# Performance work log

Hardware: AMD Instinct MI355X
Metric: run time of the kernel (lower is better)

Reference implementation:

```python
import jax, jax.numpy as jnp
import numpy as np

D = 1024      # hidden_size
FF = 4096     # ff_inner_dim = 4 * D
E = 8         # num_experts
K = 2         # moe_top_k
B, L = 4, 1024


def setup_inputs() -> dict:
    key = jax.random.key(0)
    ks = jax.random.split(key, 12)
    s = 0.02  # weight init scale
    return {
        "x": jax.random.normal(ks[0], (B, L, D), jnp.float32),
        "W_gate": jax.random.normal(ks[1], (D, E), jnp.float32) * s,
        "W1": jax.random.normal(ks[2], (E, D, FF), jnp.float32) * s,
        "b1": jnp.zeros((E, FF), jnp.float32),
        "W2": jax.random.normal(ks[3], (E, FF, D), jnp.float32) * s,
        "b2": jnp.zeros((E, D), jnp.float32),
        "Ws1": jax.random.normal(ks[4], (D, FF), jnp.float32) * s,
        "bs1": jnp.zeros((FF,), jnp.float32),
        "Ws2": jax.random.normal(ks[5], (FF, D), jnp.float32) * s,
        "bs2": jnp.zeros((D,), jnp.float32),
    }


def _gelu(h):
    # torch F.gelu default = exact (erf) gelu
    return jax.nn.gelu(h, approximate=False)


def reference(x, W_gate, W1, b1, W2, b2, Ws1, bs1, Ws2, bs2):
    Bx, Lx, Dx = x.shape
    xf = x.reshape(-1, Dx)                       # [T, D]
    logits = xf @ W_gate                         # [T, E]
    probs = jax.nn.softmax(logits, axis=-1)
    top_v, top_i = jax.lax.top_k(probs, K)       # [T, K]
    top_v = top_v / jnp.sum(top_v, axis=-1, keepdims=True)
    # dense combine weights: [T, E], zero for unselected experts
    combine = jnp.sum(jax.nn.one_hot(top_i, E, dtype=xf.dtype) * top_v[..., None], axis=1)

    out = jnp.zeros_like(xf)
    for e in range(E):  # fixed small expert loop, unrolled under jit
        h = _gelu(xf @ W1[e] + b1[e])            # [T, FF]
        out = out + combine[:, e:e + 1] * (h @ W2[e] + b2[e])

    shared = _gelu(xf @ Ws1 + bs1) @ Ws2 + bs2   # [T, D]
    return (out + shared).reshape(Bx, Lx, Dx)
```

## Files before the change

### kernel.cpp

```cpp
#include <hip/hip_runtime.h>
#include <hip/hip_bf16.h>

typedef unsigned short ushort_t;
typedef __attribute__((ext_vector_type(4))) float f32x4;
typedef __attribute__((ext_vector_type(8))) short bf16x8;
typedef __attribute__((ext_vector_type(8))) unsigned short us8;

#define T_TOK 4096
#define D_DIM 1024
#define FF_DIM 4096
#define NE 8
#define ESTRIDE 4194304L

__device__ __forceinline__ unsigned short f2bf(float f) {
  __hip_bfloat16 h = __float2bfloat16(f);
  return __builtin_bit_cast(unsigned short, h);
}
__device__ __forceinline__ float gelu_f(float v) {
  return 0.5f * v * (1.0f + erff(v * 0.70710678118654752440f));
}

__global__ void gate_kernel(const float* __restrict__ x, const float* __restrict__ Wg,
                            int* __restrict__ cnt, int* __restrict__ tok,
                            float* __restrict__ wof, int* __restrict__ rankof) {
  const int t = blockIdx.x;
  const int lane = threadIdx.x;
  const float* xr = x + (long)t * D_DIM;
  float acc[NE];
#pragma unroll
  for (int e = 0; e < NE; e++) acc[e] = 0.f;
#pragma unroll
  for (int i = 0; i < 16; i++) {
    int d = i * 64 + lane;
    float xv = xr[d];
    const float* wr = Wg + d * NE;
#pragma unroll
    for (int e = 0; e < NE; e++) acc[e] += xv * wr[e];
  }
#pragma unroll
  for (int off = 32; off > 0; off >>= 1) {
#pragma unroll
    for (int e = 0; e < NE; e++) acc[e] += __shfl_xor(acc[e], off, 64);
  }
  if (lane == 0) {
    int i0 = 0;
#pragma unroll
    for (int e = 1; e < NE; e++) if (acc[e] > acc[i0]) i0 = e;
    int i1 = -1;
#pragma unroll
    for (int e = 0; e < NE; e++) {
      if (e == i0) continue;
      if (i1 < 0 || acc[e] > acc[i1]) i1 = e;
    }
    float e1 = expf(acc[i1] - acc[i0]);
    float w0 = 1.f / (1.f + e1);
    float w1 = e1 * w0;
    int s0 = atomicAdd(&cnt[i0], 1);
    tok[i0 * T_TOK + s0] = t; wof[i0 * T_TOK + s0] = w0; rankof[i0 * T_TOK + s0] = 0;
    int s1 = atomicAdd(&cnt[i1], 1);
    tok[i1 * T_TOK + s1] = t; wof[i1 * T_TOK + s1] = w1; rankof[i1 * T_TOK + s1] = 1;
    tok[8 * T_TOK + t] = t; wof[8 * T_TOK + t] = 1.f; rankof[8 * T_TOK + t] = 0;
  }
}

__global__ void scan_kernel(int* cnt, int* base) {
  if (threadIdx.x == 0 && blockIdx.x == 0) {
    int s = 0;
    for (int e = 0; e < NE; e++) { base[e] = s; s += cnt[e]; }
    base[8] = s;
    cnt[8] = T_TOK;
  }
}

__global__ void build_queue_kernel(const int* __restrict__ cnt,
                                   unsigned int* __restrict__ q1,
                                   unsigned int* __restrict__ q2,
                                   int* __restrict__ nq) {
  const int e = blockIdx.x;
  int off1 = 0, off2 = 0, tot1 = 0, tot2 = 0, mym = 0;
  for (int i = 0; i < 9; i++) {
    int c = (i == 8) ? T_TOK : cnt[i];
    int m = (c + 127) >> 7;
    if (i < e) { off1 += m * 32; off2 += m * 8; }
    if (i == e) mym = m;
    tot1 += m * 32; tot2 += m * 8;
  }
  for (int nx = 0; nx < 32; nx++)
    for (int my = threadIdx.x; my < mym; my += 256)
      q1[off1 + nx * mym + my] = ((unsigned)e << 16) | ((unsigned)my << 8) | (unsigned)nx;
  for (int nx = 0; nx < 8; nx++)
    for (int my = threadIdx.x; my < mym; my += 256)
      q2[off2 + nx * mym + my] = ((unsigned)e << 16) | ((unsigned)my << 8) | (unsigned)nx;
  if (e == 0 && threadIdx.x == 0) { nq[0] = tot1; nq[1] = tot2; }
}

__global__ void cvt_x_kernel(const float* __restrict__ src, ushort_t* __restrict__ dst) {
  long i = ((long)blockIdx.x * 256 + threadIdx.x) * 8;
  float4 v0 = *(const float4*)(src + i);
  float4 v1 = *(const float4*)(src + i + 4);
  us8 o;
  o[0] = f2bf(v0.x); o[1] = f2bf(v0.y); o[2] = f2bf(v0.z); o[3] = f2bf(v0.w);
  o[4] = f2bf(v1.x); o[5] = f2bf(v1.y); o[6] = f2bf(v1.z); o[7] = f2bf(v1.w);
  *(us8*)(dst + i) = o;
}

__global__ void tcvt_kernel(const float* __restrict__ src, ushort_t* __restrict__ dst,
                            int R, int C) {
  src += (long)blockIdx.z * R * C;
  dst += (long)blockIdx.z * R * C;
  const int r0 = blockIdx.y * 64, c0 = blockIdx.x * 64;
  __shared__ ushort_t tile[64][72];
  const int t = threadIdx.x;
#pragma unroll
  for (int i = 0; i < 4; i++) {
    int lin = t + i * 256;
    int r = lin >> 4;
    int c = (lin & 15) * 4;
    float4 v = *(const float4*)(src + (long)(r0 + r) * C + c0 + c);
    tile[c + 0][r] = f2bf(v.x);
    tile[c + 1][r] = f2bf(v.y);
    tile[c + 2][r] = f2bf(v.z);
    tile[c + 3][r] = f2bf(v.w);
  }
  __syncthreads();
#pragma unroll
  for (int i = 0; i < 2; i++) {
    int lin = t + i * 256;
    int cc = lin >> 3, rp = lin & 7;
    us8 v = *(const us8*)&tile[cc][rp * 8];
    *(us8*)(dst + (long)(c0 + cc) * R + r0 + rp * 8) = v;
  }
}

template <int K, int N, int PHASE>
__global__ __launch_bounds__(256, 3) void gemm_kernel(
    const ushort_t* __restrict__ Abase, const ushort_t* __restrict__ WT,
    const float* __restrict__ bias_e, const float* __restrict__ bias_s,
    const int* __restrict__ cnt, const int* __restrict__ base,
    const int* __restrict__ tok, const float* __restrict__ wof,
    const int* __restrict__ rankof,
    const unsigned int* __restrict__ q, const int* __restrict__ nq_all,
    ushort_t* __restrict__ He, float* __restrict__ ybuf, float* __restrict__ out) {
  const int nq = nq_all[PHASE - 1];
  const int tid = threadIdx.x;
  const int w = tid >> 6, lane = tid & 63;
  const int wm = w >> 1, wn = w & 1;
  const int lr = lane & 15, lg = lane >> 4;

  __shared__ ushort_t lds_u[2 * 8192];
  char* const lds = (char*)lds_u;

  const int srow8 = tid >> 3;
  const int g8 = (tid & 7) ^ (srow8 & 7);

  int offA[4], offB[4];
#pragma unroll
  for (int m = 0; m < 4; m++) {
    int r = wm * 64 + m * 16 + lr;
    offA[m] = r * 128 + ((lg ^ (r & 7)) << 4);
  }
#pragma unroll
  for (int n = 0; n < 4; n++) {
    int r = wn * 64 + n * 16 + lr;
    offB[n] = r * 128 + ((lg ^ (r & 7)) << 4);
  }

  for (int it = blockIdx.x; it < nq; it += gridDim.x) {
    const unsigned int item = q[it];
    const int e = item >> 16;
    const int m0 = ((item >> 8) & 0xff) * 128;
    const int n0 = (item & 0xff) * 128;
    const int count = cnt[e];

    const ushort_t* pA[4];
    const ushort_t* pB[4];
#pragma unroll
    for (int i = 0; i < 4; i++) {
      int rr = m0 + i * 32 + srow8;
      int rc = (rr < count) ? rr : 0;
      long arow;
      if (PHASE == 1) arow = tok[e * T_TOK + rc];
      else            arow = (long)base[e] + rc;
      pA[i] = Abase + arow * (long)K + g8 * 8;
      pB[i] = WT + (long)e * ESTRIDE + (long)(n0 + i * 32 + srow8) * K + g8 * 8;
    }

    f32x4 acc[4][4] = {};

    for (int k0 = 0; k0 < K; k0 += 64) {
#pragma unroll
      for (int i = 0; i < 4; i++) {
        __builtin_amdgcn_global_load_lds(
            (const __attribute__((address_space(1))) void*)(pA[i] + k0),
            (__attribute__((address_space(3))) void*)(lds + i * 4096 + tid * 16), 16, 0, 0);
        __builtin_amdgcn_global_load_lds(
            (const __attribute__((address_space(1))) void*)(pB[i] + k0),
            (__attribute__((address_space(3))) void*)(lds + 16384 + i * 4096 + tid * 16),
            16, 0, 0);
      }
      __syncthreads();

#pragma unroll
      for (int kk = 0; kk < 2; kk++) {
        const int kx = kk << 6;
        bf16x8 av[4], bv[4];
#pragma unroll
        for (int m = 0; m < 4; m++)
          av[m] = *(const bf16x8*)(lds + (offA[m] ^ kx));
#pragma unroll
        for (int n = 0; n < 4; n++)
          bv[n] = *(const bf16x8*)(lds + 16384 + (offB[n] ^ kx));
#pragma unroll
        for (int m = 0; m < 4; m++)
#pragma unroll
          for (int n = 0; n < 4; n++)
            acc[m][n] = __builtin_amdgcn_mfma_f32_16x16x32_bf16(av[m], bv[n], acc[m][n], 0, 0, 0);
      }
      __syncthreads();
    }

    const float* bias = (e == NE) ? bias_s : (bias_e + (long)e * N);
#pragma unroll
    for (int m = 0; m < 4; m++) {
#pragma unroll
      for (int j = 0; j < 4; j++) {
        int rloc = wm * 64 + m * 16 + lg * 4 + j;
        int rr = m0 + rloc;
        if (rr >= count) continue;
        if (PHASE == 1) {
          long orow = (long)base[e] + rr;
#pragma unroll
          for (int n = 0; n < 4; n++) {
            int col = n0 + wn * 64 + n * 16 + lr;
            float v = acc[m][n][j] + bias[col];
            He[orow * FF_DIM + col] = f2bf(gelu_f(v));
          }
        } else {
          int tt = tok[e * T_TOK + rr];
          if (e == NE) {
#pragma unroll
            for (int n = 0; n < 4; n++) {
              int col = n0 + wn * 64 + n * 16 + lr;
              out[(long)tt * D_DIM + col] = acc[m][n][j] + bias[col];
            }
          } else {
            float wgt = wof[e * T_TOK + rr];
            int rk = rankof[e * T_TOK + rr];
            float* dst = ybuf + (long)rk * ((long)T_TOK * D_DIM) + (long)tt * D_DIM;
#pragma unroll
            for (int n = 0; n < 4; n++) {
              int col = n0 + wn * 64 + n * 16 + lr;
              dst[col] = wgt * (acc[m][n][j] + bias[col]);
            }
          }
        }
      }
    }
  }
}

__global__ void final_add_kernel(float* __restrict__ out, const float* __restrict__ ybuf) {
  long i = ((long)blockIdx.x * 256 + threadIdx.x) * 4;
  float4 a = *(const float4*)(out + i);
  float4 b = *(const float4*)(ybuf + i);
  float4 c = *(const float4*)(ybuf + (long)T_TOK * D_DIM + i);
  a.x += b.x + c.x; a.y += b.y + c.y; a.z += b.z + c.z; a.w += b.w + c.w;
  *(float4*)(out + i) = a;
}

extern "C" void kernel_launch(void* const* d_in, const int* in_sizes, int n_in,
                              void* d_out, int out_size, void* d_ws, size_t ws_size,
                              hipStream_t stream) {
  (void)in_sizes; (void)n_in; (void)out_size; (void)ws_size;
  const float* x   = (const float*)d_in[0];
  const float* Wg  = (const float*)d_in[1];
  const float* W1  = (const float*)d_in[2];
  const float* b1  = (const float*)d_in[3];
  const float* W2  = (const float*)d_in[4];
  const float* b2  = (const float*)d_in[5];
  const float* Ws1 = (const float*)d_in[6];
  const float* bs1 = (const float*)d_in[7];
  const float* Ws2 = (const float*)d_in[8];
  const float* bs2 = (const float*)d_in[9];
  float* out = (float*)d_out;

  char* ws = (char*)d_ws;
  int*      cnt    = (int*)(ws + 0);
  int*      base   = (int*)(ws + 64);
  int*      tok    = (int*)(ws + 256);
  float*    wof    = (float*)(ws + 256 + 147456);
  int*      rankof = (int*)(ws + 256 + 2 * 147456);
  ushort_t* Xbf    = (ushort_t*)(ws + 442624);
  ushort_t* W1T    = (ushort_t*)(ws + 8831232);
  ushort_t* W2T    = (ushort_t*)(ws + 84328704);
  ushort_t* He     = (ushort_t*)(ws + 159826176);
  int*      nq     = (int*)(ws + 260489472);
  unsigned int* q1 = (unsigned int*)(ws + 260489536);
  unsigned int* q2 = (unsigned int*)(ws + 260489536 + 32768);
  float*    ybuf   = (float*)(ws + 261538048);

  hipMemsetAsync(cnt, 0, 64, stream);
  gate_kernel<<<T_TOK, 64, 0, stream>>>(x, Wg, cnt, tok, wof, rankof);
  scan_kernel<<<1, 64, 0, stream>>>(cnt, base);
  build_queue_kernel<<<9, 256, 0, stream>>>(cnt, q1, q2, nq);
  cvt_x_kernel<<<2048, 256, 0, stream>>>(x, Xbf);
  tcvt_kernel<<<dim3(64, 16, 8), 256, 0, stream>>>(W1, W1T, 1024, 4096);
  tcvt_kernel<<<dim3(16, 64, 8), 256, 0, stream>>>(W2, W2T, 4096, 1024);
  tcvt_kernel<<<dim3(64, 16, 1), 256, 0, stream>>>(Ws1, W1T + 8L * ESTRIDE, 1024, 4096);
  tcvt_kernel<<<dim3(16, 64, 1), 256, 0, stream>>>(Ws2, W2T + 8L * ESTRIDE, 4096, 1024);
  gemm_kernel<1024, 4096, 1><<<3328, 256, 0, stream>>>(
      Xbf, W1T, b1, bs1, cnt, base, tok, wof, rankof, q1, nq, He, ybuf, out);
  gemm_kernel<4096, 1024, 2><<<832, 256, 0, stream>>>(
      He, W2T, b2, bs2, cnt, base, tok, wof, rankof, q2, nq, He, ybuf, out);
  final_add_kernel<<<4096, 256, 0, stream>>>(out, ybuf);
}
```

Baseline: 603.9 us.

## Double-buffer GEMM LDS loads, swizzle tile queue, merge weight transpose launches

The GEMM main loop now double-buffers LDS tiles. It issues the next k-slice's global_load_lds before computing the current one, using explicit vmcnt waits and barriers, and drops occupancy to 2 blocks per CU to fit the doubled LDS. The work queue is reordered into 4x8 (phase 1) and 2x2 (phase 2) tile groups, and block IDs are remapped across XCDs to improve L2 reuse of A and B tiles. The weight transpose-convert kernel handles 128-row tiles and folds the shared expert into the same launch, cutting four launches to two. The risks are reduced occupancy and the correctness of the manual waitcnt logic.

```diff
diff --git a/kernel.cpp b/kernel.cpp
--- a/kernel.cpp
+++ b/kernel.cpp
@@ -77,20 +77,28 @@
                                    unsigned int* __restrict__ q2,
                                    int* __restrict__ nq) {
   const int e = blockIdx.x;
-  int off1 = 0, off2 = 0, tot1 = 0, tot2 = 0, mym = 0;
+  int off1 = 0, off2 = 0, tot1 = 0, tot2 = 0, M = 0;
   for (int i = 0; i < 9; i++) {
     int c = (i == 8) ? T_TOK : cnt[i];
     int m = (c + 127) >> 7;
     if (i < e) { off1 += m * 32; off2 += m * 8; }
-    if (i == e) mym = m;
+    if (i == e) M = m;
     tot1 += m * 32; tot2 += m * 8;
   }
-  for (int nx = 0; nx < 32; nx++)
-    for (int my = threadIdx.x; my < mym; my += 256)
-      q1[off1 + nx * mym + my] = ((unsigned)e << 16) | ((unsigned)my << 8) | (unsigned)nx;
-  for (int nx = 0; nx < 8; nx++)
-    for (int my = threadIdx.x; my < mym; my += 256)
-      q2[off2 + nx * mym + my] = ((unsigned)e << 16) | ((unsigned)my << 8) | (unsigned)nx;
+  for (int i = threadIdx.x; i < M * 32; i += 256) {
+    int my = i >> 5, nx = i & 31;
+    int ms = my >> 2, mi = my & 3, ns = nx >> 3, ni = nx & 7;
+    int h = M - ms * 4; if (h > 4) h = 4;
+    int pos = ms * 128 + ns * (h * 8) + mi * 8 + ni;
+    q1[off1 + pos] = ((unsigned)e << 16) | ((unsigned)my << 8) | (unsigned)nx;
+  }
+  for (int i = threadIdx.x; i < M * 8; i += 256) {
+    int my = i >> 3, nx = i & 7;
+    int ms = my >> 1, mi = my & 1, ns = nx >> 1, ni = nx & 1;
+    int h = M - ms * 2; if (h > 2) h = 2;
+    int pos = ms * 16 + ns * (h * 2) + mi * 2 + ni;
+    q2[off2 + pos] = ((unsigned)e << 16) | ((unsigned)my << 8) | (unsigned)nx;
+  }
   if (e == 0 && threadIdx.x == 0) { nq[0] = tot1; nq[1] = tot2; }
 }
 
@@ -104,15 +112,15 @@
   *(us8*)(dst + i) = o;
 }
 
-__global__ void tcvt_kernel(const float* __restrict__ src, ushort_t* __restrict__ dst,
-                            int R, int C) {
-  src += (long)blockIdx.z * R * C;
-  dst += (long)blockIdx.z * R * C;
-  const int r0 = blockIdx.y * 64, c0 = blockIdx.x * 64;
-  __shared__ ushort_t tile[64][72];
+__global__ void tcvt_kernel(const float* __restrict__ W, const float* __restrict__ Wsh,
+                            ushort_t* __restrict__ dst, int R, int C) {
+  const float* src = (blockIdx.z == 8) ? Wsh : (W + (long)blockIdx.z * R * C);
+  ushort_t* d = dst + (long)blockIdx.z * R * C;
+  const int r0 = blockIdx.y * 128, c0 = blockIdx.x * 64;
+  __shared__ ushort_t tile[64][136];
   const int t = threadIdx.x;
 #pragma unroll
-  for (int i = 0; i < 4; i++) {
+  for (int i = 0; i < 8; i++) {
     int lin = t + i * 256;
     int r = lin >> 4;
     int c = (lin & 15) * 4;
@@ -124,16 +132,16 @@
   }
   __syncthreads();
 #pragma unroll
-  for (int i = 0; i < 2; i++) {
+  for (int i = 0; i < 4; i++) {
     int lin = t + i * 256;
-    int cc = lin >> 3, rp = lin & 7;
+    int cc = lin >> 4, rp = lin & 15;
     us8 v = *(const us8*)&tile[cc][rp * 8];
-    *(us8*)(dst + (long)(c0 + cc) * R + r0 + rp * 8) = v;
+    *(us8*)(d + (long)(c0 + cc) * R + r0 + rp * 8) = v;
   }
 }
 
 template <int K, int N, int PHASE>
-__global__ __launch_bounds__(256, 3) void gemm_kernel(
+__global__ __launch_bounds__(256, 2) void gemm_kernel(
     const ushort_t* __restrict__ Abase, const ushort_t* __restrict__ WT,
     const float* __restrict__ bias_e, const float* __restrict__ bias_s,
     const int* __restrict__ cnt, const int* __restrict__ base,
@@ -147,7 +155,7 @@
   const int wm = w >> 1, wn = w & 1;
   const int lr = lane & 15, lg = lane >> 4;
 
-  __shared__ ushort_t lds_u[2 * 8192];
+  __shared__ ushort_t lds_u[2 * 16384];
   char* const lds = (char*)lds_u;
 
   const int srow8 = tid >> 3;
@@ -165,7 +173,26 @@
     offB[n] = r * 128 + ((lg ^ (r & 7)) << 4);
   }
 
-  for (int it = blockIdx.x; it < nq; it += gridDim.x) {
+  constexpr int NT = K / 64;
+  const int chunk = gridDim.x >> 3;
+  const int vbid = (blockIdx.x & 7) * chunk + (blockIdx.x >> 3);
+
+#define STAGE(buf_, kk_)                                                         \
+  do {                                                                           \
+    char* dd_ = lds + (buf_) * 32768 + tid * 16;                                 \
+    _Pragma("unroll")                                                            \
+    for (int i_ = 0; i_ < 4; i_++) {                                             \
+      __builtin_amdgcn_global_load_lds(                                          \
+          (const __attribute__((address_space(1))) void*)(pA[i_] + (kk_)),       \
+          (__attribute__((address_space(3))) void*)(dd_ + i_ * 4096), 16, 0, 0); \
+      __builtin_amdgcn_global_load_lds(                                          \
+          (const __attribute__((address_space(1))) void*)(pB[i_] + (kk_)),       \
+          (__attribute__((address_space(3))) void*)(dd_ + 16384 + i_ * 4096),    \
+          16, 0, 0);                                                             \
+    }                                                                            \
+  } while (0)
+
+  for (int it = vbid; it < nq; it += gridDim.x) {
     const unsigned int item = q[it];
     const int e = item >> 16;
     const int m0 = ((item >> 8) & 0xff) * 128;
@@ -187,36 +214,40 @@
 
     f32x4 acc[4][4] = {};
 
-    for (int k0 = 0; k0 < K; k0 += 64) {
-#pragma unroll
-      for (int i = 0; i < 4; i++) {
-        __builtin_amdgcn_global_load_lds(
-            (const __attribute__((address_space(1))) void*)(pA[i] + k0),
-            (__attribute__((address_space(3))) void*)(lds + i * 4096 + tid * 16), 16, 0, 0);
-        __builtin_amdgcn_global_load_lds(
-            (const __attribute__((address_space(1))) void*)(pB[i] + k0),
-            (__attribute__((address_space(3))) void*)(lds + 16384 + i * 4096 + tid * 16),
-            16, 0, 0);
+    __builtin_amdgcn_s_barrier();
+    asm volatile("" ::: "memory");
+    STAGE(0, 0);
+
+    for (int t = 0; t < NT; t++) {
+      if (t + 1 < NT) {
+        STAGE((t + 1) & 1, (t + 1) * 64);
+        asm volatile("s_waitcnt vmcnt(8)" ::: "memory");
+      } else {
+        asm volatile("s_waitcnt vmcnt(0)" ::: "memory");
       }
-      __syncthreads();
-
+      __builtin_amdgcn_s_barrier();
+      asm volatile("" ::: "memory");
+
+      const char* aB = lds + (t & 1) * 32768;
+      const char* bB = aB + 16384;
 #pragma unroll
       for (int kk = 0; kk < 2; kk++) {
         const int kx = kk << 6;
         bf16x8 av[4], bv[4];
 #pragma unroll
         for (int m = 0; m < 4; m++)
-          av[m] = *(const bf16x8*)(lds + (offA[m] ^ kx));
+          av[m] = *(const bf16x8*)(aB + (offA[m] ^ kx));
 #pragma unroll
         for (int n = 0; n < 4; n++)
-          bv[n] = *(const bf16x8*)(lds + 16384 + (offB[n] ^ kx));
+          bv[n] = *(const bf16x8*)(bB + (offB[n] ^ kx));
 #pragma unroll
         for (int m = 0; m < 4; m++)
 #pragma unroll
           for (int n = 0; n < 4; n++)
             acc[m][n] = __builtin_amdgcn_mfma_f32_16x16x32_bf16(av[m], bv[n], acc[m][n], 0, 0, 0);
       }
-      __syncthreads();
+      __builtin_amdgcn_s_barrier();
+      asm volatile("" ::: "memory");
     }
 
     const float* bias = (e == NE) ? bias_s : (bias_e + (long)e * N);
@@ -257,6 +288,7 @@
       }
     }
   }
+#undef STAGE
 }
 
 __global__ void final_add_kernel(float* __restrict__ out, const float* __restrict__ ybuf) {
@@ -304,10 +336,8 @@
   scan_kernel<<<1, 64, 0, stream>>>(cnt, base);
   build_queue_kernel<<<9, 256, 0, stream>>>(cnt, q1, q2, nq);
   cvt_x_kernel<<<2048, 256, 0, stream>>>(x, Xbf);
-  tcvt_kernel<<<dim3(64, 16, 8), 256, 0, stream>>>(W1, W1T, 1024, 4096);
-  tcvt_kernel<<<dim3(16, 64, 8), 256, 0, stream>>>(W2, W2T, 4096, 1024);
-  tcvt_kernel<<<dim3(64, 16, 1), 256, 0, stream>>>(Ws1, W1T + 8L * ESTRIDE, 1024, 4096);
-  tcvt_kernel<<<dim3(16, 64, 1), 256, 0, stream>>>(Ws2, W2T + 8L * ESTRIDE, 4096, 1024);
+  tcvt_kernel<<<dim3(64, 8, 9), 256, 0, stream>>>(W1, Ws1, W1T, 1024, 4096);
+  tcvt_kernel<<<dim3(16, 32, 9), 256, 0, stream>>>(W2, Ws2, W2T, 4096, 1024);
   gemm_kernel<1024, 4096, 1><<<3328, 256, 0, stream>>>(
       Xbf, W1T, b1, bs1, cnt, base, tok, wof, rankof, q1, nq, He, ybuf, out);
   gemm_kernel<4096, 1024, 2><<<832, 256, 0, stream>>>(
```

New measurement: 547.9 us. 1.1x faster.
